# Optimization experiments

Hardware: AMD Instinct MI355X
Metric: run time of the kernel (lower is better)

Reference implementation:

```python
import jax, jax.numpy as jnp
import numpy as np

N = 100000       # num nodes
E = 1600000      # num edges
D_IN = 32
D_HID = 32
D_OUT = 32
K = 3            # Chebyshev order (number of terms)


def setup_inputs() -> dict:
    key = jax.random.key(0)
    k1, k2, k3, k4, k5, k6 = jax.random.split(key, 6)
    x = jax.random.normal(k1, (N, D_IN), dtype=jnp.float32)
    edge_index = jax.random.randint(k2, (2, E), 0, N, dtype=jnp.int64)
    s1 = 1.0 / np.sqrt(D_IN)
    s2 = 1.0 / np.sqrt(D_HID)
    W1 = jax.random.uniform(k3, (K, D_IN, D_HID), jnp.float32, -s1, s1)
    b1 = jax.random.uniform(k4, (D_HID,), jnp.float32, -s1, s1)
    W2 = jax.random.uniform(k5, (K, D_HID, D_OUT), jnp.float32, -s2, s2)
    b2 = jax.random.uniform(k6, (D_OUT,), jnp.float32, -s2, s2)
    return {"x": x, "edge_index": edge_index, "W1": W1, "b1": b1, "W2": W2, "b2": b2}


def _prop(x, row, col, w):
    # L_hat @ x : gather along col, scale by edge weight, scatter-add to row.
    # (diagonal of the rescaled Laplacian cancels to 0 in PyG ChebConv with
    #  sym normalization and lambda_max=2, so only off-diagonal edges remain)
    return jax.ops.segment_sum(w[:, None] * x[col], row, num_segments=N)


def _cheb_conv(x, row, col, w, W, b):
    # Chebyshev recurrence: Tx0 = x, Tx1 = L_hat x, Tx_k = 2 L_hat Tx_{k-1} - Tx_{k-2}
    k_terms = W.shape[0]
    Tx0 = x
    out = Tx0 @ W[0]
    if k_terms > 1:
        Tx1 = _prop(Tx0, row, col, w)
        out = out + Tx1 @ W[1]
        for k in range(2, k_terms):
            Tx2 = 2.0 * _prop(Tx1, row, col, w) - Tx0
            out = out + Tx2 @ W[k]
            Tx0, Tx1 = Tx1, Tx2
    return out + b


def reference(x, edge_index, W1, b1, W2, b2):
    row, col = edge_index[0], edge_index[1]
    mask = (row != col).astype(x.dtype)            # remove_self_loops
    deg = jax.ops.segment_sum(mask, row, num_segments=N)
    dinv = jnp.where(deg > 0, 1.0 / jnp.sqrt(jnp.maximum(deg, 1.0)), 0.0)
    w = -mask * dinv[row] * dinv[col]              # scaled Laplacian off-diagonal weights
    x0 = x
    h = jax.nn.relu(_cheb_conv(x, row, col, w, W1, b1))
    h = _cheb_conv(h, row, col, w, W2, b2)
    return h + x0
```

## Files before the change

kernel.cpp:

```cpp
#include <hip/hip_runtime.h>

#define NN 100000
#define EE 1600000
#define DD 32
#define NBUK 391
#define BROWS 256
#define TILE 4096
#define NT 391
#define BCAP2 4864

typedef unsigned int uint;
typedef unsigned short ushort;
typedef unsigned char uchar;
typedef __attribute__((ext_vector_type(8))) short bf16x8;
typedef __attribute__((ext_vector_type(4))) float f32x4;

typedef __attribute__((ext_vector_type(4))) uint u32x4v;
typedef __attribute__((ext_vector_type(2))) uint u32x2v;
typedef __attribute__((ext_vector_type(2))) int i32x2v;
typedef __attribute__((ext_vector_type(4))) float f32x4v;

__device__ __forceinline__ uint4 ntld(const uint4* p) {
    u32x4v v = __builtin_nontemporal_load((const u32x4v*)p);
    uint4 r; r.x = v.x; r.y = v.y; r.z = v.z; r.w = v.w; return r;
}
__device__ __forceinline__ uint2 ntld(const uint2* p) {
    u32x2v v = __builtin_nontemporal_load((const u32x2v*)p);
    uint2 r; r.x = v.x; r.y = v.y; return r;
}
__device__ __forceinline__ int2 ntld(const int2* p) {
    i32x2v v = __builtin_nontemporal_load((const i32x2v*)p);
    int2 r; r.x = v.x; r.y = v.y; return r;
}
__device__ __forceinline__ float4 ntld(const float4* p) {
    f32x4v v = __builtin_nontemporal_load((const f32x4v*)p);
    float4 r; r.x = v.x; r.y = v.y; r.z = v.z; r.w = v.w; return r;
}
__device__ __forceinline__ int   ntld(const int* p)   { return __builtin_nontemporal_load(p); }
__device__ __forceinline__ float ntld(const float* p) { return __builtin_nontemporal_load(p); }
__device__ __forceinline__ void ntst(uint4* p, uint4 v) {
    u32x4v w; w.x = v.x; w.y = v.y; w.z = v.z; w.w = v.w;
    __builtin_nontemporal_store(w, (u32x4v*)p);
}
__device__ __forceinline__ void ntst(uint2* p, uint2 v) {
    u32x2v w; w.x = v.x; w.y = v.y;
    __builtin_nontemporal_store(w, (u32x2v*)p);
}
__device__ __forceinline__ void ntst(int* p, int v)     { __builtin_nontemporal_store(v, p); }
__device__ __forceinline__ void ntst(float* p, float v) { __builtin_nontemporal_store(v, p); }

__device__ __forceinline__ ushort f2b(float f) {
    uint u = __float_as_uint(f);
    u += 0x7fffu + ((u >> 16) & 1u);
    return (ushort)(u >> 16);
}
__device__ __forceinline__ float b2f(ushort h) {
    return __uint_as_float((uint)h << 16);
}
__device__ __forceinline__ uint f2e4(float f) {
    uint u = __float_as_uint(f);
    uint s = (u >> 24) & 0x80u;
    float a = fabsf(f) * 0x1p-120f;
    uint g = __float_as_uint(a);
    g += 0x7FFFFu + ((g >> 20) & 1u);
    uint m = g >> 20;
    if (m > 0x7Eu) m = 0x7Eu;
    return s | m;
}
__device__ __forceinline__ bf16x8 as_bf16x8(uint4 v) {
    union { uint4 u; bf16x8 b; } cv; cv.u = v; return cv.b;
}
__device__ __forceinline__ void acc8(float* acc, uint2 v) {
#pragma unroll
    for (int wi = 0; wi < 2; ++wi) {
        uint w = (&v.x)[wi];
        acc[wi * 4 + 0] += 0x1p120f * __uint_as_float(((w & 0x80u) << 24) | ((w & 0x7fu) << 20));
        acc[wi * 4 + 1] += 0x1p120f * __uint_as_float(((w & 0x8000u) << 16) | ((w & 0x7f00u) << 12));
        acc[wi * 4 + 2] += 0x1p120f * __uint_as_float(((w & 0x800000u) << 8) | ((w & 0x7f0000u) << 4));
        acc[wi * 4 + 3] += 0x1p120f * __uint_as_float((w & 0x80000000u) | ((w & 0x7f000000u) >> 4));
    }
}


__global__ void k_part(const int* __restrict__ ei, int* __restrict__ gtail,
                       int* __restrict__ pairs) {
    __shared__ int hist[512];
    __shared__ int gbase[512];
    int t = threadIdx.x;
    hist[t] = 0; hist[t + 256] = 0;
    __syncthreads();
    int e0 = blockIdx.x * TILE;
    int pk[16], rk[16], bb[16];
#pragma unroll
    for (int k = 0; k < 16; ++k) {
        int e = e0 + t + k * 256;
        bb[k] = -1;
        if (e < EE) {
            int r = ntld(ei + e), c = ntld(ei + EE + e);
            if (r != c) {
                bb[k] = r >> 8;
                pk[k] = (r & (BROWS - 1)) | (c << 8);
                rk[k] = atomicAdd(&hist[bb[k]], 1);
            }
        }
    }
    __syncthreads();
    for (int q = t; q < NBUK; q += 256) {
        int cnt = hist[q];
        gbase[q] = cnt ? atomicAdd(&gtail[q * 16], cnt) : 0;
    }
    __syncthreads();
#pragma unroll
    for (int k = 0; k < 16; ++k) {
        if (bb[k] >= 0) {
            int pos = gbase[bb[k]] + rk[k];
            if (pos < BCAP2) pairs[bb[k] * BCAP2 + pos] = pk[k];
        }
    }
}


__global__ void k_build2(const int* __restrict__ gtail, const int* __restrict__ pairs,
                         float* __restrict__ dinv, int* __restrict__ desc,
                         int* __restrict__ ghist, int* __restrict__ ent) {
    __shared__ int lcnt[BROWS];
    __shared__ int lh[16];
    __shared__ int slab[BROWS * 64];
    int b = blockIdx.x, t = threadIdx.x;
    lcnt[t] = 0;
    if (t < 16) lh[t] = 0;
    for (int i = t; i < BROWS * 64; i += 256) slab[i] = NN;
    __syncthreads();
    int cnt = gtail[b * 16]; if (cnt > BCAP2) cnt = BCAP2;
    const int* pp = pairs + b * BCAP2;
    for (int i = t; i < cnt; i += 256) {
        int v = ntld(pp + i);
        int lr = v & (BROWS - 1);
        int pos = atomicAdd(&lcnt[lr], 1);
        if (pos < 64) slab[(lr << 6) + pos] = (int)((uint)v >> 8);
    }
    __syncthreads();
    {
        int n = b * BROWS + t;
        if (n < NN) {
            int d = lcnt[t];
            int ms = d > 64 ? 64 : d;
            int cls = (ms + 7) >> 3;
            dinv[n] = d > 0 ? rsqrtf((float)d) : 0.0f;
            desc[n] = (n << 3) | (cls << 24);
            atomicAdd(&lh[cls], 1);
        }
    }
    __syncthreads();
    if (t < 16 && lh[t]) atomicAdd(&ghist[t], lh[t]);
    int base = b * (BROWS * 64);
    for (int i = t; i < BROWS * 64; i += 256)
        ntst(ent + base + i, slab[i]);
}


__global__ void k_perms(const int* __restrict__ desc, int* __restrict__ classcur,
                        int2* __restrict__ pdesc) {
    __shared__ int h[16];
    __shared__ int base[16];
    if (threadIdx.x < 16) h[threadIdx.x] = 0;
    __syncthreads();
    int n = blockIdx.x * blockDim.x + threadIdx.x;
    int d = 0, cls = 0, rk = 0;
    if (n < NN) {
        d = desc[n];
        cls = (d >> 24) & 15;
        rk = atomicAdd(&h[cls], 1);
    }
    __syncthreads();
    if (threadIdx.x < 16 && h[threadIdx.x])
        base[threadIdx.x] = atomicAdd(&classcur[threadIdx.x], h[threadIdx.x]);
    __syncthreads();
    if (n < NN) {
        int2 v; v.x = n; v.y = d;
        pdesc[base[cls] + rk] = v;
    }
}


__global__ void k_cvt(const float* __restrict__ x, uint2* __restrict__ xb,
                      uint* __restrict__ xb8, const float* __restrict__ dinv,
                      const float* __restrict__ W1, const float* __restrict__ W2,
                      ushort* __restrict__ wb1, ushort* __restrict__ wb2,
                      const int* __restrict__ ghist, int* __restrict__ classcur,
                      uint* __restrict__ t1b8, uint* __restrict__ hb8) {
    if (blockIdx.x == (NN * DD / 4) / 256) {
        for (int i = threadIdx.x; i < 6144; i += 256) {
            const float* W = W1; ushort* wb = wb1;
            int ii = i;
            if (ii >= 3072) { ii -= 3072; W = W2; wb = wb2; }
            int term = ii >> 10, rem = ii & 1023;
            int h = rem >> 9, lane = (rem >> 3) & 63, j = rem & 7;
            int k = ((lane >> 4) << 3) + j;
            int col = (h << 4) | (lane & 15);
            wb[ii] = f2b(W[term * 1024 + k * 32 + col]);
        }
        return;
    }
    if (blockIdx.x == 0) {
        if (threadIdx.x == 0) {
            int s = 0;
            for (int i = 0; i < 16; ++i) { classcur[i] = s; s += ghist[i]; }
        }
        if (threadIdx.x >= 64 && threadIdx.x < 72) xb8[NN * 8 + threadIdx.x - 64] = 0;
        if (threadIdx.x >= 72 && threadIdx.x < 80) t1b8[NN * 8 + threadIdx.x - 72] = 0;
        if (threadIdx.x >= 80 && threadIdx.x < 88) hb8[NN * 8 + threadIdx.x - 80] = 0;
    }
    int tid = blockIdx.x * blockDim.x + threadIdx.x;
    if (tid >= NN * DD / 4) return;
    float4 v = ntld(((const float4*)x) + tid);
    uint2 b;
    b.x = (uint)f2b(v.x) | ((uint)f2b(v.y) << 16);
    b.y = (uint)f2b(v.z) | ((uint)f2b(v.w) << 16);
    ntst(xb + tid, b);
    float dv = dinv[tid >> 3];
    xb8[tid] = f2e4(dv * v.x) | (f2e4(dv * v.y) << 8)
             | (f2e4(dv * v.z) << 16) | (f2e4(dv * v.w) << 24);
}


__global__ void k_prop(const int2* __restrict__ pdesc, const int* __restrict__ ent,
                       const float* __restrict__ dinv,
                       const uint2* __restrict__ src8d,
                       const uint4* __restrict__ baseq,
                       uint2* __restrict__ dst8d,
                       uint4* __restrict__ dstbq,
                       float alpha, float beta) {
    int tid = blockIdx.x * blockDim.x + threadIdx.x;
    int g = tid >> 3;
    if (g >= NN) return;
    int sub = tid & 3, h = (tid >> 2) & 1;
    int2 pd = ntld(pdesc + g);
    int n = pd.x;
    const int* ep = ent + ((size_t)(pd.y & 0xFFFFFF) << 3);
    int mr = ((pd.y >> 24) & 15) << 3;
    float acc[8] = {0, 0, 0, 0, 0, 0, 0, 0};
    for (int i = h * 8; i < mr; i += 16) {
        uint4 C0 = ntld((const uint4*)(ep + i));
        uint4 C1 = ntld((const uint4*)(ep + i + 4));
        uint2 v0 = src8d[(C0.x << 2) + sub];
        uint2 v1 = src8d[(C0.y << 2) + sub];
        uint2 v2 = src8d[(C0.z << 2) + sub];
        uint2 v3 = src8d[(C0.w << 2) + sub];
        uint2 v4 = src8d[(C1.x << 2) + sub];
        uint2 v5 = src8d[(C1.y << 2) + sub];
        uint2 v6 = src8d[(C1.z << 2) + sub];
        uint2 v7 = src8d[(C1.w << 2) + sub];
        acc8(acc, v0);
        acc8(acc, v1);
        acc8(acc, v2);
        acc8(acc, v3);
        acc8(acc, v4);
        acc8(acc, v5);
        acc8(acc, v6);
        acc8(acc, v7);
    }
    float dn = dinv[n];
    float s = -alpha * dn;
#pragma unroll
    for (int k = 0; k < 8; ++k)
        acc[k] = s * (acc[k] + __shfl_xor(acc[k], 4, 64));
    if (baseq) {
        uint4 b = ntld(baseq + (n << 2) + sub);
#pragma unroll
        for (int wi = 0; wi < 4; ++wi) {
            uint w = (&b.x)[wi];
            acc[wi * 2 + 0] += beta * __uint_as_float(w << 16);
            acc[wi * 2 + 1] += beta * __uint_as_float(w & 0xffff0000u);
        }
    }
    if (h == 0) {
        uint4 ob;
#pragma unroll
        for (int wi = 0; wi < 4; ++wi)
            (&ob.x)[wi] = (uint)f2b(acc[wi * 2]) | ((uint)f2b(acc[wi * 2 + 1]) << 16);
        ntst(dstbq + (n << 2) + sub, ob);
    } else if (dst8d) {
        uint2 o8;
        o8.x = f2e4(dn * acc[0]) | (f2e4(dn * acc[1]) << 8)
             | (f2e4(dn * acc[2]) << 16) | (f2e4(dn * acc[3]) << 24);
        o8.y = f2e4(dn * acc[4]) | (f2e4(dn * acc[5]) << 8)
             | (f2e4(dn * acc[6]) << 16) | (f2e4(dn * acc[7]) << 24);
        ntst(dst8d + (n << 2) + sub, o8);
    }
}


__global__ void k_comb(const uint4* __restrict__ t0, const uint4* __restrict__ t1,
                       const uint4* __restrict__ t2, const ushort* __restrict__ wb,
                       const float* __restrict__ bias, const float* __restrict__ residf,
                       const float* __restrict__ dinv,
                       float* __restrict__ outf, ushort* __restrict__ outb,
                       uchar* __restrict__ outb8, int do_relu) {
    int lane = threadIdx.x & 63;
    int wid = threadIdx.x >> 6;
    int n0 = (blockIdx.x * 4 + wid) << 6;
    if (n0 >= NN) return;
    int q = lane >> 4, lr = lane & 15;
    const uint4* wq = (const uint4*)wb;
    bf16x8 bf[3][2];
#pragma unroll
    for (int t = 0; t < 3; ++t)
#pragma unroll
        for (int h = 0; h < 2; ++h)
            bf[t][h] = as_bf16x8(wq[((t * 2 + h) << 6) + lane]);
    float bias0 = bias[lr], bias1 = bias[16 + lr];
    uint4 z; z.x = 0; z.y = 0; z.z = 0; z.w = 0;
#pragma unroll
    for (int mt = 0; mt < 4; ++mt) {
        int nb = n0 + (mt << 4);
        int row = nb + lr;
        bool ok = row < NN;
        int ai = (row << 2) + q;
        bf16x8 a0 = as_bf16x8(ok ? ntld(t0 + ai) : z);
        bf16x8 a1 = as_bf16x8(ok ? ntld(t1 + ai) : z);
        bf16x8 a2 = as_bf16x8(ok ? ntld(t2 + ai) : z);
        f32x4 c0 = {0.f, 0.f, 0.f, 0.f};
        f32x4 c1 = {0.f, 0.f, 0.f, 0.f};
        c0 = __builtin_amdgcn_mfma_f32_16x16x32_bf16(a0, bf[0][0], c0, 0, 0, 0);
        c0 = __builtin_amdgcn_mfma_f32_16x16x32_bf16(a1, bf[1][0], c0, 0, 0, 0);
        c0 = __builtin_amdgcn_mfma_f32_16x16x32_bf16(a2, bf[2][0], c0, 0, 0, 0);
        c1 = __builtin_amdgcn_mfma_f32_16x16x32_bf16(a0, bf[0][1], c1, 0, 0, 0);
        c1 = __builtin_amdgcn_mfma_f32_16x16x32_bf16(a1, bf[1][1], c1, 0, 0, 0);
        c1 = __builtin_amdgcn_mfma_f32_16x16x32_bf16(a2, bf[2][1], c1, 0, 0, 0);
#pragma unroll
        for (int r = 0; r < 4; ++r) {
            int node = nb + (q << 2) + r;
            if (node >= NN) continue;
            float v0 = c0[r] + bias0;
            float v1 = c1[r] + bias1;
            if (do_relu) { v0 = fmaxf(v0, 0.0f); v1 = fmaxf(v1, 0.0f); }
            if (outb) {
                float dv = dinv[node];
                outb[node * DD + lr] = f2b(v0);
                outb[node * DD + 16 + lr] = f2b(v1);
                outb8[node * DD + lr] = (uchar)f2e4(dv * v0);
                outb8[node * DD + 16 + lr] = (uchar)f2e4(dv * v1);
            } else {
                ntst(outf + node * DD + lr, v0 + ntld(residf + node * DD + lr));
                ntst(outf + node * DD + 16 + lr, v1 + ntld(residf + node * DD + 16 + lr));
            }
        }
    }
}


extern "C" void kernel_launch(void* const* d_in, const int* in_sizes, int n_in,
                              void* d_out, int out_size, void* d_ws, size_t ws_size,
                              hipStream_t stream) {
    const float* x  = (const float*)d_in[0];
    const int*   ei = (const int*)d_in[1];
    const float* W1 = (const float*)d_in[2];
    const float* b1 = (const float*)d_in[3];
    const float* W2 = (const float*)d_in[4];
    const float* b2 = (const float*)d_in[5];
    float* out = (float*)d_out;

    char* wsp = (char*)d_ws;
    size_t off = 0;
    auto take = [&](size_t bytes) {
        char* p = wsp + off;
        off = (off + bytes + 255) & ~(size_t)255;
        return p;
    };
    int*    ctrl  = (int*)take((size_t)(NBUK * 16 + 32) * 4);
    int*    gtail = ctrl;
    int*    ghist = ctrl + NBUK * 16;
    int*    ccur  = ctrl + NBUK * 16 + 16;
    float*  dinv  = (float*)take((size_t)NN * 4);
    int*    desc  = (int*)take((size_t)NN * 4);
    int2*   pdesc = (int2*)take((size_t)NN * 8);
    ushort* wb1   = (ushort*)take((size_t)3072 * 2);
    ushort* wb2   = (ushort*)take((size_t)3072 * 2);
    int*    pairs = (int*)take((size_t)NBUK * BCAP2 * 4);
    int*    ent   = (int*)take((size_t)NBUK * BROWS * 64 * 4);
    ushort* xb    = (ushort*)take((size_t)NN * DD * 2);
    ushort* t1b   = (ushort*)take((size_t)NN * DD * 2);
    ushort* t2b   = (ushort*)take((size_t)NN * DD * 2);
    ushort* hb    = (ushort*)take((size_t)NN * DD * 2);
    uchar*  xb8   = (uchar*)take((size_t)(NN + 1) * DD);
    uchar*  t1b8  = (uchar*)take((size_t)(NN + 1) * DD);
    uchar*  hb8   = (uchar*)take((size_t)(NN + 1) * DD);

    hipMemsetAsync(ctrl, 0, (size_t)(NBUK * 16 + 32) * 4, stream);

    k_part  <<<NT, 256, 0, stream>>>(ei, gtail, pairs);
    k_build2<<<NBUK, 256, 0, stream>>>(gtail, pairs, dinv, desc, ghist, ent);
    k_cvt   <<<NN * DD / 4 / 256 + 1, 256, 0, stream>>>(x, (uint2*)xb, (uint*)xb8, dinv,
                                                        W1, W2, wb1, wb2, ghist, ccur,
                                                        (uint*)t1b8, (uint*)hb8);
    k_perms <<<(NN + 255) / 256, 256, 0, stream>>>(desc, ccur, pdesc);

    const int pgrid = (NN * 8 + 255) / 256;
    const int mgrid = (NN + 255) / 256;
    k_prop<<<pgrid, 256, 0, stream>>>(pdesc, ent, dinv, (const uint2*)xb8, nullptr,
                                      (uint2*)t1b8, (uint4*)t1b, 1.0f, 0.0f);
    k_prop<<<pgrid, 256, 0, stream>>>(pdesc, ent, dinv, (const uint2*)t1b8,
                                      (const uint4*)xb, nullptr, (uint4*)t2b, 2.0f, -1.0f);
    k_comb<<<mgrid, 256, 0, stream>>>((const uint4*)xb, (const uint4*)t1b,
                                      (const uint4*)t2b, wb1, b1, nullptr, dinv,
                                      nullptr, hb, hb8, 1);
    k_prop<<<pgrid, 256, 0, stream>>>(pdesc, ent, dinv, (const uint2*)hb8, nullptr,
                                      (uint2*)t1b8, (uint4*)t1b, 1.0f, 0.0f);
    k_prop<<<pgrid, 256, 0, stream>>>(pdesc, ent, dinv, (const uint2*)t1b8,
                                      (const uint4*)hb, nullptr, (uint4*)t2b, 2.0f, -1.0f);
    k_comb<<<mgrid, 256, 0, stream>>>((const uint4*)hb, (const uint4*)t1b,
                                      (const uint4*)t2b, wb2, b2, x, dinv,
                                      out, nullptr, nullptr, 0);
}
```

Measured before the change: 251.5 us.

## Fuse second Chebyshev propagation with weight combine and fold conversion into build

```diff
diff --git a/kernel.cpp b/kernel.cpp
--- a/kernel.cpp
+++ b/kernel.cpp
@@ -46,6 +46,10 @@
     u32x2v w; w.x = v.x; w.y = v.y;
     __builtin_nontemporal_store(w, (u32x2v*)p);
 }
+__device__ __forceinline__ void ntst(float4* p, float4 v) {
+    f32x4v w; w.x = v.x; w.y = v.y; w.z = v.z; w.w = v.w;
+    __builtin_nontemporal_store(w, (f32x4v*)p);
+}
 __device__ __forceinline__ void ntst(int* p, int v)     { __builtin_nontemporal_store(v, p); }
 __device__ __forceinline__ void ntst(float* p, float v) { __builtin_nontemporal_store(v, p); }
 
@@ -53,9 +57,6 @@
     uint u = __float_as_uint(f);
     u += 0x7fffu + ((u >> 16) & 1u);
     return (ushort)(u >> 16);
-}
-__device__ __forceinline__ float b2f(ushort h) {
-    return __uint_as_float((uint)h << 16);
 }
 __device__ __forceinline__ uint f2e4(float f) {
     uint u = __float_as_uint(f);
@@ -70,6 +71,14 @@
 __device__ __forceinline__ bf16x8 as_bf16x8(uint4 v) {
     union { uint4 u; bf16x8 b; } cv; cv.u = v; return cv.b;
 }
+__device__ __forceinline__ void dec8(float* v, uint4 q) {
+#pragma unroll
+    for (int wi = 0; wi < 4; ++wi) {
+        uint w = (&q.x)[wi];
+        v[wi * 2 + 0] = __uint_as_float(w << 16);
+        v[wi * 2 + 1] = __uint_as_float(w & 0xffff0000u);
+    }
+}
 __device__ __forceinline__ void acc8(float* acc, uint2 v) {
 #pragma unroll
     for (int wi = 0; wi < 2; ++wi) {
@@ -83,7 +92,15 @@
 
 
 __global__ void k_part(const int* __restrict__ ei, int* __restrict__ gtail,
-                       int* __restrict__ pairs) {
+                       int* __restrict__ pairs, uint* __restrict__ xb8,
+                       uint* __restrict__ t1b8, uint* __restrict__ hb8) {
+    if (blockIdx.x == NT) {
+        int t = threadIdx.x;
+        if (t < 8) xb8[NN * 8 + t] = 0;
+        else if (t < 16) t1b8[NN * 8 + t - 8] = 0;
+        else if (t < 24) hb8[NN * 8 + t - 16] = 0;
+        return;
+    }
     __shared__ int hist[512];
     __shared__ int gbase[512];
     int t = threadIdx.x;
@@ -122,9 +139,13 @@
 
 __global__ void k_build2(const int* __restrict__ gtail, const int* __restrict__ pairs,
                          float* __restrict__ dinv, int* __restrict__ desc,
-                         int* __restrict__ ghist, int* __restrict__ ent) {
+                         int* __restrict__ ghist, int* __restrict__ ent,
+                         const float* __restrict__ x, uint2* __restrict__ xb,
+                         uint* __restrict__ xb8, int* __restrict__ classcur,
+                         int* __restrict__ done) {
     __shared__ int lcnt[BROWS];
     __shared__ int lh[16];
+    __shared__ float sdinv[BROWS];
     __shared__ int slab[BROWS * 64];
     int b = blockIdx.x, t = threadIdx.x;
     lcnt[t] = 0;
@@ -142,20 +163,49 @@
     __syncthreads();
     {
         int n = b * BROWS + t;
+        float dv = 0.0f;
         if (n < NN) {
             int d = lcnt[t];
             int ms = d > 64 ? 64 : d;
             int cls = (ms + 7) >> 3;
-            dinv[n] = d > 0 ? rsqrtf((float)d) : 0.0f;
+            dv = d > 0 ? rsqrtf((float)d) : 0.0f;
+            dinv[n] = dv;
             desc[n] = (n << 3) | (cls << 24);
             atomicAdd(&lh[cls], 1);
         }
+        sdinv[t] = dv;
     }
     __syncthreads();
     if (t < 16 && lh[t]) atomicAdd(&ghist[t], lh[t]);
+    int base4 = b * 2048;
+    for (int i = t; i < 2048; i += 256) {
+        int row = i >> 3;
+        if (b * BROWS + row < NN) {
+            float4 v = ntld((const float4*)x + base4 + i);
+            uint2 b2;
+            b2.x = (uint)f2b(v.x) | ((uint)f2b(v.y) << 16);
+            b2.y = (uint)f2b(v.z) | ((uint)f2b(v.w) << 16);
+            ntst(xb + base4 + i, b2);
+            float dv = sdinv[row];
+            xb8[base4 + i] = f2e4(dv * v.x) | (f2e4(dv * v.y) << 8)
+                           | (f2e4(dv * v.z) << 16) | (f2e4(dv * v.w) << 24);
+        }
+    }
     int base = b * (BROWS * 64);
     for (int i = t; i < BROWS * 64; i += 256)
         ntst(ent + base + i, slab[i]);
+    __syncthreads();
+    if (t == 0) {
+        __threadfence();
+        if (atomicAdd(done, 1) == NBUK - 1) {
+            int s = 0;
+#pragma unroll
+            for (int i = 0; i < 16; ++i) {
+                int c = atomicAdd(&ghist[i], 0);
+                classcur[i] = s; s += c;
+            }
+        }
+    }
 }
 
 
@@ -183,54 +233,11 @@
 }
 
 
-__global__ void k_cvt(const float* __restrict__ x, uint2* __restrict__ xb,
-                      uint* __restrict__ xb8, const float* __restrict__ dinv,
-                      const float* __restrict__ W1, const float* __restrict__ W2,
-                      ushort* __restrict__ wb1, ushort* __restrict__ wb2,
-                      const int* __restrict__ ghist, int* __restrict__ classcur,
-                      uint* __restrict__ t1b8, uint* __restrict__ hb8) {
-    if (blockIdx.x == (NN * DD / 4) / 256) {
-        for (int i = threadIdx.x; i < 6144; i += 256) {
-            const float* W = W1; ushort* wb = wb1;
-            int ii = i;
-            if (ii >= 3072) { ii -= 3072; W = W2; wb = wb2; }
-            int term = ii >> 10, rem = ii & 1023;
-            int h = rem >> 9, lane = (rem >> 3) & 63, j = rem & 7;
-            int k = ((lane >> 4) << 3) + j;
-            int col = (h << 4) | (lane & 15);
-            wb[ii] = f2b(W[term * 1024 + k * 32 + col]);
-        }
-        return;
-    }
-    if (blockIdx.x == 0) {
-        if (threadIdx.x == 0) {
-            int s = 0;
-            for (int i = 0; i < 16; ++i) { classcur[i] = s; s += ghist[i]; }
-        }
-        if (threadIdx.x >= 64 && threadIdx.x < 72) xb8[NN * 8 + threadIdx.x - 64] = 0;
-        if (threadIdx.x >= 72 && threadIdx.x < 80) t1b8[NN * 8 + threadIdx.x - 72] = 0;
-        if (threadIdx.x >= 80 && threadIdx.x < 88) hb8[NN * 8 + threadIdx.x - 80] = 0;
-    }
-    int tid = blockIdx.x * blockDim.x + threadIdx.x;
-    if (tid >= NN * DD / 4) return;
-    float4 v = ntld(((const float4*)x) + tid);
-    uint2 b;
-    b.x = (uint)f2b(v.x) | ((uint)f2b(v.y) << 16);
-    b.y = (uint)f2b(v.z) | ((uint)f2b(v.w) << 16);
-    ntst(xb + tid, b);
-    float dv = dinv[tid >> 3];
-    xb8[tid] = f2e4(dv * v.x) | (f2e4(dv * v.y) << 8)
-             | (f2e4(dv * v.z) << 16) | (f2e4(dv * v.w) << 24);
-}
-
-
 __global__ void k_prop(const int2* __restrict__ pdesc, const int* __restrict__ ent,
                        const float* __restrict__ dinv,
                        const uint2* __restrict__ src8d,
-                       const uint4* __restrict__ baseq,
                        uint2* __restrict__ dst8d,
-                       uint4* __restrict__ dstbq,
-                       float alpha, float beta) {
+                       uint4* __restrict__ dstbq) {
     int tid = blockIdx.x * blockDim.x + threadIdx.x;
     int g = tid >> 3;
     if (g >= NN) return;
@@ -251,36 +258,21 @@
         uint2 v5 = src8d[(C1.y << 2) + sub];
         uint2 v6 = src8d[(C1.z << 2) + sub];
         uint2 v7 = src8d[(C1.w << 2) + sub];
-        acc8(acc, v0);
-        acc8(acc, v1);
-        acc8(acc, v2);
-        acc8(acc, v3);
-        acc8(acc, v4);
-        acc8(acc, v5);
-        acc8(acc, v6);
-        acc8(acc, v7);
+        acc8(acc, v0); acc8(acc, v1); acc8(acc, v2); acc8(acc, v3);
+        acc8(acc, v4); acc8(acc, v5); acc8(acc, v6); acc8(acc, v7);
     }
     float dn = dinv[n];
-    float s = -alpha * dn;
+    float s = -dn;
 #pragma unroll
     for (int k = 0; k < 8; ++k)
         acc[k] = s * (acc[k] + __shfl_xor(acc[k], 4, 64));
-    if (baseq) {
-        uint4 b = ntld(baseq + (n << 2) + sub);
-#pragma unroll
-        for (int wi = 0; wi < 4; ++wi) {
-            uint w = (&b.x)[wi];
-            acc[wi * 2 + 0] += beta * __uint_as_float(w << 16);
-            acc[wi * 2 + 1] += beta * __uint_as_float(w & 0xffff0000u);
-        }
-    }
     if (h == 0) {
         uint4 ob;
 #pragma unroll
         for (int wi = 0; wi < 4; ++wi)
             (&ob.x)[wi] = (uint)f2b(acc[wi * 2]) | ((uint)f2b(acc[wi * 2 + 1]) << 16);
         ntst(dstbq + (n << 2) + sub, ob);
-    } else if (dst8d) {
+    } else {
         uint2 o8;
         o8.x = f2e4(dn * acc[0]) | (f2e4(dn * acc[1]) << 8)
              | (f2e4(dn * acc[2]) << 16) | (f2e4(dn * acc[3]) << 24);
@@ -291,59 +283,119 @@
 }
 
 
-__global__ void k_comb(const uint4* __restrict__ t0, const uint4* __restrict__ t1,
-                       const uint4* __restrict__ t2, const ushort* __restrict__ wb,
-                       const float* __restrict__ bias, const float* __restrict__ residf,
-                       const float* __restrict__ dinv,
-                       float* __restrict__ outf, ushort* __restrict__ outb,
-                       uchar* __restrict__ outb8, int do_relu) {
-    int lane = threadIdx.x & 63;
-    int wid = threadIdx.x >> 6;
-    int n0 = (blockIdx.x * 4 + wid) << 6;
-    if (n0 >= NN) return;
-    int q = lane >> 4, lr = lane & 15;
-    const uint4* wq = (const uint4*)wb;
-    bf16x8 bf[3][2];
-#pragma unroll
-    for (int t = 0; t < 3; ++t)
-#pragma unroll
-        for (int h = 0; h < 2; ++h)
-            bf[t][h] = as_bf16x8(wq[((t * 2 + h) << 6) + lane]);
-    float bias0 = bias[lr], bias1 = bias[16 + lr];
-    uint4 z; z.x = 0; z.y = 0; z.z = 0; z.w = 0;
-#pragma unroll
-    for (int mt = 0; mt < 4; ++mt) {
-        int nb = n0 + (mt << 4);
-        int row = nb + lr;
-        bool ok = row < NN;
-        int ai = (row << 2) + q;
-        bf16x8 a0 = as_bf16x8(ok ? ntld(t0 + ai) : z);
-        bf16x8 a1 = as_bf16x8(ok ? ntld(t1 + ai) : z);
-        bf16x8 a2 = as_bf16x8(ok ? ntld(t2 + ai) : z);
-        f32x4 c0 = {0.f, 0.f, 0.f, 0.f};
-        f32x4 c1 = {0.f, 0.f, 0.f, 0.f};
-        c0 = __builtin_amdgcn_mfma_f32_16x16x32_bf16(a0, bf[0][0], c0, 0, 0, 0);
-        c0 = __builtin_amdgcn_mfma_f32_16x16x32_bf16(a1, bf[1][0], c0, 0, 0, 0);
-        c0 = __builtin_amdgcn_mfma_f32_16x16x32_bf16(a2, bf[2][0], c0, 0, 0, 0);
-        c1 = __builtin_amdgcn_mfma_f32_16x16x32_bf16(a0, bf[0][1], c1, 0, 0, 0);
-        c1 = __builtin_amdgcn_mfma_f32_16x16x32_bf16(a1, bf[1][1], c1, 0, 0, 0);
-        c1 = __builtin_amdgcn_mfma_f32_16x16x32_bf16(a2, bf[2][1], c1, 0, 0, 0);
-#pragma unroll
-        for (int r = 0; r < 4; ++r) {
-            int node = nb + (q << 2) + r;
-            if (node >= NN) continue;
-            float v0 = c0[r] + bias0;
-            float v1 = c1[r] + bias1;
-            if (do_relu) { v0 = fmaxf(v0, 0.0f); v1 = fmaxf(v1, 0.0f); }
-            if (outb) {
-                float dv = dinv[node];
-                outb[node * DD + lr] = f2b(v0);
-                outb[node * DD + 16 + lr] = f2b(v1);
-                outb8[node * DD + lr] = (uchar)f2e4(dv * v0);
-                outb8[node * DD + 16 + lr] = (uchar)f2e4(dv * v1);
-            } else {
-                ntst(outf + node * DD + lr, v0 + ntld(residf + node * DD + lr));
-                ntst(outf + node * DD + 16 + lr, v1 + ntld(residf + node * DD + 16 + lr));
+__global__ void __launch_bounds__(256) k_prop2c(
+        const int2* __restrict__ pdesc, const int* __restrict__ ent,
+        const float* __restrict__ dinv,
+        const uint2* __restrict__ src8d,
+        const uint4* __restrict__ baseq,
+        const uint4* __restrict__ t1tab,
+        const float* __restrict__ W,
+        const float* __restrict__ bias,
+        const float* __restrict__ residf,
+        float* __restrict__ outf,
+        uint4* __restrict__ outb,
+        uint4* __restrict__ outb8,
+        int do_relu) {
+    __shared__ float ws[3072 + 32];
+    for (int i = threadIdx.x; i < 3072; i += 256) {
+        int t = i >> 10, r = i & 1023, j = r >> 5, k = r & 31;
+        ws[i] = W[(t << 10) + (k << 5) + j];
+    }
+    if (threadIdx.x < 32) ws[3072 + threadIdx.x] = bias[threadIdx.x];
+    __syncthreads();
+    int tid = blockIdx.x * blockDim.x + threadIdx.x;
+    int g = tid >> 3;
+    if (g >= NN) return;
+    int sub = tid & 3, h = (tid >> 2) & 1;
+    int2 pd = ntld(pdesc + g);
+    int n = pd.x;
+    const int* ep = ent + ((size_t)(pd.y & 0xFFFFFF) << 3);
+    int mr = ((pd.y >> 24) & 15) << 3;
+    float acc[8] = {0, 0, 0, 0, 0, 0, 0, 0};
+    for (int i = h * 8; i < mr; i += 16) {
+        uint4 C0 = ntld((const uint4*)(ep + i));
+        uint4 C1 = ntld((const uint4*)(ep + i + 4));
+        uint2 v0 = src8d[(C0.x << 2) + sub];
+        uint2 v1 = src8d[(C0.y << 2) + sub];
+        uint2 v2 = src8d[(C0.z << 2) + sub];
+        uint2 v3 = src8d[(C0.w << 2) + sub];
+        uint2 v4 = src8d[(C1.x << 2) + sub];
+        uint2 v5 = src8d[(C1.y << 2) + sub];
+        uint2 v6 = src8d[(C1.z << 2) + sub];
+        uint2 v7 = src8d[(C1.w << 2) + sub];
+        acc8(acc, v0); acc8(acc, v1); acc8(acc, v2); acc8(acc, v3);
+        acc8(acc, v4); acc8(acc, v5); acc8(acc, v6); acc8(acc, v7);
+    }
+    float dn = dinv[n];
+    float s = -2.0f * dn;
+#pragma unroll
+    for (int k = 0; k < 8; ++k)
+        acc[k] = s * (acc[k] + __shfl_xor(acc[k], 4, 64));
+    uint4 b4 = ntld(baseq + (n << 2) + sub);
+    float x0[8]; dec8(x0, b4);
+#pragma unroll
+    for (int k = 0; k < 8; ++k) acc[k] -= x0[k];
+    uint4 t1v = ntld(t1tab + (n << 2) + sub);
+    float p[16];
+#pragma unroll
+    for (int j = 0; j < 16; ++j) p[j] = 0.0f;
+#pragma unroll
+    for (int t = 0; t < 3; ++t) {
+        float v[8];
+        if (t == 0) {
+#pragma unroll
+            for (int k = 0; k < 8; ++k) v[k] = x0[k];
+        } else if (t == 1) {
+            dec8(v, t1v);
+        } else {
+#pragma unroll
+            for (int k = 0; k < 8; ++k) v[k] = acc[k];
+        }
+        const float* wb = ws + (((t << 5) + (h << 4)) << 5) + (sub << 3);
+#pragma unroll
+        for (int j = 0; j < 16; ++j) {
+            const float* wp = wb + (j << 5);
+            float4 w0 = *(const float4*)wp;
+            float4 w1 = *(const float4*)(wp + 4);
+            p[j] += v[0] * w0.x + v[1] * w0.y + v[2] * w0.z + v[3] * w0.w
+                  + v[4] * w1.x + v[5] * w1.y + v[6] * w1.z + v[7] * w1.w;
+        }
+    }
+#pragma unroll
+    for (int j = 0; j < 16; ++j) {
+        p[j] += __shfl_xor(p[j], 1, 64);
+        p[j] += __shfl_xor(p[j], 2, 64);
+        p[j] += ws[3072 + (h << 4) + j];
+        if (do_relu) p[j] = fmaxf(p[j], 0.0f);
+    }
+    if (outb) {
+        if (sub == 0) {
+            uint4 o0, o1;
+#pragma unroll
+            for (int wi = 0; wi < 4; ++wi) {
+                (&o0.x)[wi] = (uint)f2b(p[wi * 2]) | ((uint)f2b(p[wi * 2 + 1]) << 16);
+                (&o1.x)[wi] = (uint)f2b(p[8 + wi * 2]) | ((uint)f2b(p[8 + wi * 2 + 1]) << 16);
+            }
+            ntst(outb + (n << 2) + (h << 1), o0);
+            ntst(outb + (n << 2) + (h << 1) + 1, o1);
+        } else if (sub == 1) {
+            uint4 o8;
+#pragma unroll
+            for (int wi = 0; wi < 4; ++wi)
+                (&o8.x)[wi] = f2e4(dn * p[wi * 4]) | (f2e4(dn * p[wi * 4 + 1]) << 8)
+                            | (f2e4(dn * p[wi * 4 + 2]) << 16) | (f2e4(dn * p[wi * 4 + 3]) << 24);
+            ntst(outb8 + (n << 1) + h, o8);
+        }
+    } else {
+        if (sub == 0) {
+            int bi = (n << 5) + (h << 4);
+#pragma unroll
+            for (int jj = 0; jj < 4; ++jj) {
+                float4 r = ntld((const float4*)(residf + bi) + jj);
+                float4 o;
+                o.x = p[jj * 4 + 0] + r.x; o.y = p[jj * 4 + 1] + r.y;
+                o.z = p[jj * 4 + 2] + r.z; o.w = p[jj * 4 + 3] + r.w;
+                ntst((float4*)(outf + bi) + jj, o);
             }
         }
     }
@@ -368,48 +420,42 @@
         off = (off + bytes + 255) & ~(size_t)255;
         return p;
     };
-    int*    ctrl  = (int*)take((size_t)(NBUK * 16 + 32) * 4);
+    int*    ctrl  = (int*)take((size_t)(NBUK * 16 + 48) * 4);
     int*    gtail = ctrl;
     int*    ghist = ctrl + NBUK * 16;
     int*    ccur  = ctrl + NBUK * 16 + 16;
+    int*    done  = ctrl + NBUK * 16 + 32;
     float*  dinv  = (float*)take((size_t)NN * 4);
     int*    desc  = (int*)take((size_t)NN * 4);
     int2*   pdesc = (int2*)take((size_t)NN * 8);
-    ushort* wb1   = (ushort*)take((size_t)3072 * 2);
-    ushort* wb2   = (ushort*)take((size_t)3072 * 2);
     int*    pairs = (int*)take((size_t)NBUK * BCAP2 * 4);
     int*    ent   = (int*)take((size_t)NBUK * BROWS * 64 * 4);
     ushort* xb    = (ushort*)take((size_t)NN * DD * 2);
     ushort* t1b   = (ushort*)take((size_t)NN * DD * 2);
-    ushort* t2b   = (ushort*)take((size_t)NN * DD * 2);
     ushort* hb    = (ushort*)take((size_t)NN * DD * 2);
     uchar*  xb8   = (uchar*)take((size_t)(NN + 1) * DD);
     uchar*  t1b8  = (uchar*)take((size_t)(NN + 1) * DD);
     uchar*  hb8   = (uchar*)take((size_t)(NN + 1) * DD);
 
-    hipMemsetAsync(ctrl, 0, (size_t)(NBUK * 16 + 32) * 4, stream);
-
-    k_part  <<<NT, 256, 0, stream>>>(ei, gtail, pairs);
-    k_build2<<<NBUK, 256, 0, stream>>>(gtail, pairs, dinv, desc, ghist, ent);
-    k_cvt   <<<NN * DD / 4 / 256 + 1, 256, 0, stream>>>(x, (uint2*)xb, (uint*)xb8, dinv,
-                                                        W1, W2, wb1, wb2, ghist, ccur,
-                                                        (uint*)t1b8, (uint*)hb8);
+    hipMemsetAsync(ctrl, 0, (size_t)(NBUK * 16 + 48) * 4, stream);
+
+    k_part  <<<NT + 1, 256, 0, stream>>>(ei, gtail, pairs,
+                                         (uint*)xb8, (uint*)t1b8, (uint*)hb8);
+    k_build2<<<NBUK, 256, 0, stream>>>(gtail, pairs, dinv, desc, ghist, ent,
+                                       x, (uint2*)xb, (uint*)xb8, ccur, done);
     k_perms <<<(NN + 255) / 256, 256, 0, stream>>>(desc, ccur, pdesc);
 
     const int pgrid = (NN * 8 + 255) / 256;
-    const int mgrid = (NN + 255) / 256;
-    k_prop<<<pgrid, 256, 0, stream>>>(pdesc, ent, dinv, (const uint2*)xb8, nullptr,
-                                      (uint2*)t1b8, (uint4*)t1b, 1.0f, 0.0f);
-    k_prop<<<pgrid, 256, 0, stream>>>(pdesc, ent, dinv, (const uint2*)t1b8,
-                                      (const uint4*)xb, nullptr, (uint4*)t2b, 2.0f, -1.0f);
-    k_comb<<<mgrid, 256, 0, stream>>>((const uint4*)xb, (const uint4*)t1b,
-                                      (const uint4*)t2b, wb1, b1, nullptr, dinv,
-                                      nullptr, hb, hb8, 1);
-    k_prop<<<pgrid, 256, 0, stream>>>(pdesc, ent, dinv, (const uint2*)hb8, nullptr,
-                                      (uint2*)t1b8, (uint4*)t1b, 1.0f, 0.0f);
-    k_prop<<<pgrid, 256, 0, stream>>>(pdesc, ent, dinv, (const uint2*)t1b8,
-                                      (const uint4*)hb, nullptr, (uint4*)t2b, 2.0f, -1.0f);
-    k_comb<<<mgrid, 256, 0, stream>>>((const uint4*)hb, (const uint4*)t1b,
-                                      (const uint4*)t2b, wb2, b2, x, dinv,
-                                      out, nullptr, nullptr, 0);
-}
+    k_prop  <<<pgrid, 256, 0, stream>>>(pdesc, ent, dinv, (const uint2*)xb8,
+                                        (uint2*)t1b8, (uint4*)t1b);
+    k_prop2c<<<pgrid, 256, 0, stream>>>(pdesc, ent, dinv, (const uint2*)t1b8,
+                                        (const uint4*)xb, (const uint4*)t1b,
+                                        W1, b1, nullptr, nullptr,
+                                        (uint4*)hb, (uint4*)hb8, 1);
+    k_prop  <<<pgrid, 256, 0, stream>>>(pdesc, ent, dinv, (const uint2*)hb8,
+                                        (uint2*)t1b8, (uint4*)t1b);
+    k_prop2c<<<pgrid, 256, 0, stream>>>(pdesc, ent, dinv, (const uint2*)t1b8,
+                                        (const uint4*)hb, (const uint4*)t1b,
+                                        W2, b2, x, out,
+                                        nullptr, nullptr, 0);
+}
```

After: 300.1 us. 1.19x slower.

## Fold the -Tx0 Chebyshev term into W0 and decode fp8 with hardware conversions

Applied to the files above, without the earlier changes.

```diff
diff --git a/kernel.cpp b/kernel.cpp
--- a/kernel.cpp
+++ b/kernel.cpp
@@ -14,6 +14,7 @@
 typedef unsigned char uchar;
 typedef __attribute__((ext_vector_type(8))) short bf16x8;
 typedef __attribute__((ext_vector_type(4))) float f32x4;
+typedef __attribute__((ext_vector_type(2))) float f32x2;
 
 typedef __attribute__((ext_vector_type(4))) uint u32x4v;
 typedef __attribute__((ext_vector_type(2))) uint u32x2v;
@@ -53,9 +54,6 @@
     uint u = __float_as_uint(f);
     u += 0x7fffu + ((u >> 16) & 1u);
     return (ushort)(u >> 16);
-}
-__device__ __forceinline__ float b2f(ushort h) {
-    return __uint_as_float((uint)h << 16);
 }
 __device__ __forceinline__ uint f2e4(float f) {
     uint u = __float_as_uint(f);
@@ -74,10 +72,12 @@
 #pragma unroll
     for (int wi = 0; wi < 2; ++wi) {
         uint w = (&v.x)[wi];
-        acc[wi * 4 + 0] += 0x1p120f * __uint_as_float(((w & 0x80u) << 24) | ((w & 0x7fu) << 20));
-        acc[wi * 4 + 1] += 0x1p120f * __uint_as_float(((w & 0x8000u) << 16) | ((w & 0x7f00u) << 12));
-        acc[wi * 4 + 2] += 0x1p120f * __uint_as_float(((w & 0x800000u) << 8) | ((w & 0x7f0000u) << 4));
-        acc[wi * 4 + 3] += 0x1p120f * __uint_as_float((w & 0x80000000u) | ((w & 0x7f000000u) >> 4));
+        f32x2 lo = __builtin_amdgcn_cvt_pk_f32_fp8((int)w, false);
+        f32x2 hi = __builtin_amdgcn_cvt_pk_f32_fp8((int)w, true);
+        acc[wi * 4 + 0] += lo.x;
+        acc[wi * 4 + 1] += lo.y;
+        acc[wi * 4 + 2] += hi.x;
+        acc[wi * 4 + 3] += hi.y;
     }
 }
 
@@ -198,7 +198,9 @@
             int h = rem >> 9, lane = (rem >> 3) & 63, j = rem & 7;
             int k = ((lane >> 4) << 3) + j;
             int col = (h << 4) | (lane & 15);
-            wb[ii] = f2b(W[term * 1024 + k * 32 + col]);
+            float val = W[term * 1024 + k * 32 + col];
+            if (term == 0) val -= W[2 * 1024 + k * 32 + col];
+            wb[ii] = f2b(val);
         }
         return;
     }
@@ -227,10 +229,9 @@
 __global__ void k_prop(const int2* __restrict__ pdesc, const int* __restrict__ ent,
                        const float* __restrict__ dinv,
                        const uint2* __restrict__ src8d,
-                       const uint4* __restrict__ baseq,
                        uint2* __restrict__ dst8d,
                        uint4* __restrict__ dstbq,
-                       float alpha, float beta) {
+                       float alpha) {
     int tid = blockIdx.x * blockDim.x + threadIdx.x;
     int g = tid >> 3;
     if (g >= NN) return;
@@ -251,29 +252,14 @@
         uint2 v5 = src8d[(C1.y << 2) + sub];
         uint2 v6 = src8d[(C1.z << 2) + sub];
         uint2 v7 = src8d[(C1.w << 2) + sub];
-        acc8(acc, v0);
-        acc8(acc, v1);
-        acc8(acc, v2);
-        acc8(acc, v3);
-        acc8(acc, v4);
-        acc8(acc, v5);
-        acc8(acc, v6);
-        acc8(acc, v7);
+        acc8(acc, v0); acc8(acc, v1); acc8(acc, v2); acc8(acc, v3);
+        acc8(acc, v4); acc8(acc, v5); acc8(acc, v6); acc8(acc, v7);
     }
     float dn = dinv[n];
     float s = -alpha * dn;
 #pragma unroll
     for (int k = 0; k < 8; ++k)
         acc[k] = s * (acc[k] + __shfl_xor(acc[k], 4, 64));
-    if (baseq) {
-        uint4 b = ntld(baseq + (n << 2) + sub);
-#pragma unroll
-        for (int wi = 0; wi < 4; ++wi) {
-            uint w = (&b.x)[wi];
-            acc[wi * 2 + 0] += beta * __uint_as_float(w << 16);
-            acc[wi * 2 + 1] += beta * __uint_as_float(w & 0xffff0000u);
-        }
-    }
     if (h == 0) {
         uint4 ob;
 #pragma unroll
@@ -398,17 +384,17 @@
 
     const int pgrid = (NN * 8 + 255) / 256;
     const int mgrid = (NN + 255) / 256;
-    k_prop<<<pgrid, 256, 0, stream>>>(pdesc, ent, dinv, (const uint2*)xb8, nullptr,
-                                      (uint2*)t1b8, (uint4*)t1b, 1.0f, 0.0f);
+    k_prop<<<pgrid, 256, 0, stream>>>(pdesc, ent, dinv, (const uint2*)xb8,
+                                      (uint2*)t1b8, (uint4*)t1b, 1.0f);
     k_prop<<<pgrid, 256, 0, stream>>>(pdesc, ent, dinv, (const uint2*)t1b8,
-                                      (const uint4*)xb, nullptr, (uint4*)t2b, 2.0f, -1.0f);
+                                      nullptr, (uint4*)t2b, 2.0f);
     k_comb<<<mgrid, 256, 0, stream>>>((const uint4*)xb, (const uint4*)t1b,
                                       (const uint4*)t2b, wb1, b1, nullptr, dinv,
                                       nullptr, hb, hb8, 1);
-    k_prop<<<pgrid, 256, 0, stream>>>(pdesc, ent, dinv, (const uint2*)hb8, nullptr,
-                                      (uint2*)t1b8, (uint4*)t1b, 1.0f, 0.0f);
+    k_prop<<<pgrid, 256, 0, stream>>>(pdesc, ent, dinv, (const uint2*)hb8,
+                                      (uint2*)t1b8, (uint4*)t1b, 1.0f);
     k_prop<<<pgrid, 256, 0, stream>>>(pdesc, ent, dinv, (const uint2*)t1b8,
-                                      (const uint4*)hb, nullptr, (uint4*)t2b, 2.0f, -1.0f);
+                                      nullptr, (uint4*)t2b, 2.0f);
     k_comb<<<mgrid, 256, 0, stream>>>((const uint4*)hb, (const uint4*)t1b,
                                       (const uint4*)t2b, wb2, b2, x, dinv,
                                       out, nullptr, nullptr, 0);
```

Result: faster. 239.9 us (-4.6%).
